# Kernel optimization log

Measured on AMD Instinct MI355X. Metric: run time of the kernel, lower is better.

The kernel has to match this reference:

```python
import jax, jax.numpy as jnp
import numpy as np

HEADS = 16
HEAD_DIM = 64
EMB = HEADS * HEAD_DIM
MAX_REL = 512
B, L = 4, 1024


def _rel_indices(length_q, length_k):
    # Shaw-style clipped relative distance indices into the embeddings table
    dist = jnp.arange(length_k)[None, :] - jnp.arange(length_q)[:, None]
    return jnp.clip(dist, -MAX_REL, MAX_REL) + MAX_REL  # [Lq, Lk] in [0, 2*MAX_REL]


def setup_inputs() -> dict:
    key = jax.random.key(0)
    ks = jax.random.split(key, 16)
    d = {
        "query": jax.random.normal(ks[0], (B, L, EMB), jnp.float32),
        "key": jax.random.normal(ks[1], (B, L, EMB), jnp.float32),
        "value": jax.random.normal(ks[2], (B, L, EMB), jnp.float32),
        "mask": jnp.ones((B, 1, L, L), jnp.int32),
        # per-head Linear(head_dims, head_dims) weights stored torch-style [out, in]
        "Wq": jax.random.normal(ks[3], (HEAD_DIM, HEAD_DIM), jnp.float32) / np.sqrt(HEAD_DIM),
        "bq": jax.random.normal(ks[4], (HEAD_DIM,), jnp.float32) * 0.02,
        "Wk": jax.random.normal(ks[5], (HEAD_DIM, HEAD_DIM), jnp.float32) / np.sqrt(HEAD_DIM),
        "bk": jax.random.normal(ks[6], (HEAD_DIM,), jnp.float32) * 0.02,
        "Wv": jax.random.normal(ks[7], (HEAD_DIM, HEAD_DIM), jnp.float32) / np.sqrt(HEAD_DIM),
        "bv": jax.random.normal(ks[8], (HEAD_DIM,), jnp.float32) * 0.02,
        "Wfc": jax.random.normal(ks[9], (EMB, EMB), jnp.float32) / np.sqrt(EMB),
        "bfc": jax.random.normal(ks[10], (EMB,), jnp.float32) * 0.02,
        "rel_k_table": jax.random.normal(ks[11], (2 * MAX_REL + 1, HEAD_DIM), jnp.float32) * 0.02,
        "rel_v_table": jax.random.normal(ks[12], (2 * MAX_REL + 1, HEAD_DIM), jnp.float32) * 0.02,
    }
    return d


def reference(query, key, value, mask, Wq, bq, Wk, bk, Wv, bv, Wfc, bfc, rel_k_table, rel_v_table):
    b, lq, _ = query.shape
    lk = key.shape[1]
    # split heads then per-head linear projections (torch Linear: x @ W.T + b)
    q = query.reshape(b, lq, HEADS, HEAD_DIM) @ Wq.T + bq
    k = key.reshape(b, lk, HEADS, HEAD_DIM) @ Wk.T + bk
    v = value.reshape(b, lk, HEADS, HEAD_DIM) @ Wv.T + bv

    score = jnp.einsum('bqhd,bkhd->bhqk', q, k)  # [B,H,Lq,Lk]
    score = jnp.where(mask == 0, jnp.float32(-1e20), score)

    idx = _rel_indices(lq, lk)
    a_key = rel_k_table[idx]    # [Lq, Lk, D]
    a_val = rel_v_table[idx]    # [Lq, Lk, D]
    score = score + jnp.einsum('blhd,lrd->bhlr', q, a_key)

    attn = jax.nn.softmax(score / np.sqrt(HEAD_DIM), axis=-1)

    out = jnp.einsum('bhqv,bvhd->bqhd', attn, v)
    # original: einsum('brhl,hld->bhrd', attn[b,h,q,k], a_val[q,k,d]) -> [b,q,h,d]
    out = out + jnp.einsum('bhql,qld->bqhd', attn, a_val)
    out = out.reshape(b, lq, EMB)
    return out @ Wfc.T + bfc
```

## Files before the change

kernel.cpp:

```cpp
#include <hip/hip_runtime.h>
#include <hip/hip_bf16.h>
#include <hip/hip_fp16.h>

#define SEQ 1024
#define HEADS 16
#define HDIM 64
#define EMB 1024
#define TQ 32
#define KQ 256
#define PBA_S 264
#define PBB_S 328
#define RELK_ROWS 1040
#define RELV_S 1064

typedef __bf16 bf16x8 __attribute__((ext_vector_type(8)));
typedef float floatx4 __attribute__((ext_vector_type(4)));
typedef unsigned short u16x4 __attribute__((ext_vector_type(4)));

#if __has_builtin(__builtin_amdgcn_exp2f)
#define EXP2F(x) __builtin_amdgcn_exp2f(x)
#else
#define EXP2F(x) exp2f(x)
#endif

#define QSCALE 0.18033688011112042f

static __device__ __forceinline__ unsigned short f2bu(float f) {
    __bf16 h = (__bf16)f;
    return __builtin_bit_cast(unsigned short, h);
}
static __device__ __forceinline__ float b2f(unsigned short u) {
    unsigned v = ((unsigned)u) << 16;
    return __builtin_bit_cast(float, v);
}

__global__ __launch_bounds__(256) void sa_proj_kernel(
    const float* __restrict__ qin, const float* __restrict__ kin,
    const float* __restrict__ vin,
    const unsigned short* __restrict__ wqb, const unsigned short* __restrict__ wkb,
    const unsigned short* __restrict__ wvb,
    const float* __restrict__ bq, const float* __restrict__ bk,
    const float* __restrict__ bv_,
    unsigned short* __restrict__ qb, unsigned short* __restrict__ kb,
    unsigned short* __restrict__ vtb,
    const unsigned* __restrict__ part, unsigned* __restrict__ flags) {
    const int t = threadIdx.x;
    if (blockIdx.x == 0 && blockIdx.y == 0 && t < 4) {
        unsigned f = 0xFFFFFFFFu;
        for (int i = 0; i < 64; ++i) f &= part[t * 64 + i];
        flags[t] = f;
    }
    const int w = t >> 6, lane = t & 63;
    const int quad = lane >> 4, l16 = lane & 15;
    const int which = blockIdx.y;
    const int bx = blockIdx.x;
    const int r0 = (bx >> 2) * 16;
    const int h = (bx & 3) * 4 + w;
    const int bidx = r0 >> 10;
    const int l0 = r0 & 1023;
    const float* x = (which == 0) ? qin : (which == 1) ? kin : vin;
    const unsigned short* Wb = (which == 0) ? wqb : (which == 1) ? wkb : wvb;
    const float* bias = (which == 0) ? bq : (which == 1) ? bk : bv_;

    bf16x8 wf[4][2];
#pragma unroll
    for (int dt = 0; dt < 4; ++dt)
#pragma unroll
        for (int ks = 0; ks < 2; ++ks)
            wf[dt][ks] = *(const bf16x8*)(Wb + (size_t)(dt * 16 + l16) * 64 + ks * 32 + quad * 8);

    bf16x8 xf[2];
#pragma unroll
    for (int ks = 0; ks < 2; ++ks) {
        const float* xp = x + (size_t)(r0 + l16) * EMB + h * 64 + ks * 32 + quad * 8;
        float4 lo = *(const float4*)xp;
        float4 hi = *(const float4*)(xp + 4);
        unsigned short px[8];
        px[0] = f2bu(lo.x); px[1] = f2bu(lo.y); px[2] = f2bu(lo.z); px[3] = f2bu(lo.w);
        px[4] = f2bu(hi.x); px[5] = f2bu(hi.y); px[6] = f2bu(hi.z); px[7] = f2bu(hi.w);
        xf[ks] = *(bf16x8*)px;
    }
    const int bh = bidx * HEADS + h;

    if (which < 2) {
        float biasd[4];
#pragma unroll
        for (int dt = 0; dt < 4; ++dt) biasd[dt] = bias[dt * 16 + l16];
        const float sc = (which == 0) ? QSCALE : 1.0f;
        unsigned short* dst = (which == 0) ? qb : kb;
        floatx4 acc[4];
#pragma unroll
        for (int dt = 0; dt < 4; ++dt) acc[dt] = floatx4{0.f, 0.f, 0.f, 0.f};
#pragma unroll
        for (int dt = 0; dt < 4; ++dt)
#pragma unroll
            for (int ks = 0; ks < 2; ++ks)
                acc[dt] = __builtin_amdgcn_mfma_f32_16x16x32_bf16(xf[ks], wf[dt][ks], acc[dt], 0, 0, 0);
#pragma unroll
        for (int dt = 0; dt < 4; ++dt)
#pragma unroll
            for (int i = 0; i < 4; ++i) {
                const int lr = l0 + quad * 4 + i;
                float val = (acc[dt][i] + biasd[dt]) * sc;
                dst[((size_t)bh * SEQ + lr) * 64 + dt * 16 + l16] = f2bu(val);
            }
    } else {
        float biasv[4][4];
#pragma unroll
        for (int dt = 0; dt < 4; ++dt)
#pragma unroll
            for (int i = 0; i < 4; ++i) biasv[dt][i] = bias[dt * 16 + quad * 4 + i];
        floatx4 acc[4];
#pragma unroll
        for (int dt = 0; dt < 4; ++dt) acc[dt] = floatx4{0.f, 0.f, 0.f, 0.f};
#pragma unroll
        for (int dt = 0; dt < 4; ++dt)
#pragma unroll
            for (int ks = 0; ks < 2; ++ks)
                acc[dt] = __builtin_amdgcn_mfma_f32_16x16x32_bf16(wf[dt][ks], xf[ks], acc[dt], 0, 0, 0);
#pragma unroll
        for (int dt = 0; dt < 4; ++dt)
#pragma unroll
            for (int i = 0; i < 4; ++i) {
                const int d = dt * 16 + quad * 4 + i;
                float val = acc[dt][i] + biasv[dt][i];
                vtb[((size_t)bh * 64 + d) * SEQ + l0 + l16] = f2bu(val);
            }
    }
}

#define NW (1024 * 1024)
#define NRK (RELK_ROWS * 64)
#define NRV (64 * RELV_S)
#define NWP (3 * 4096)
#define CONV_BLOCKS ((NW + NRK + NRV + NWP) / 256)
__global__ __launch_bounds__(256) void sa_prep_kernel(
    const float* __restrict__ Wfc, const float* __restrict__ relk,
    const float* __restrict__ relv,
    const float* __restrict__ Wq, const float* __restrict__ Wk,
    const float* __restrict__ Wv, const int* __restrict__ mask,
    unsigned short* __restrict__ wfcb, unsigned short* __restrict__ relkb,
    unsigned short* __restrict__ relvtb,
    unsigned short* __restrict__ wqb, unsigned short* __restrict__ wkb,
    unsigned short* __restrict__ wvb, unsigned* __restrict__ part) {
    const int bx = blockIdx.x;
    const int t = threadIdx.x;
    if (bx < CONV_BLOCKS) {
        int i = bx * 256 + t;
        if (i < NW) {
            wfcb[i] = f2bu(Wfc[i]);
        } else if (i < NW + NRK) {
            int j = i - NW;
            int r = j >> 6, d = j & 63;
            relkb[j] = (r <= 1024) ? f2bu(relk[r * 64 + d]) : 0;
        } else if (i < NW + NRK + NRV) {
            int j = i - NW - NRK;
            int d = j / RELV_S, c = j - d * RELV_S;
            relvtb[j] = (c <= 1024) ? f2bu(relv[c * 64 + d]) : 0;
        } else {
            int j = i - NW - NRK - NRV;
            int which = j >> 12, e = j & 4095;
            const float* src = (which == 0) ? Wq : (which == 1) ? Wk : Wv;
            unsigned short* dst = (which == 0) ? wqb : (which == 1) ? wkb : wvb;
            dst[e] = f2bu(src[e]);
        }
    } else {
        const int mb = bx - CONV_BLOCKS;
        const int b = mb >> 6, chunk = mb & 63;
        const int4* p = (const int4*)(mask + (size_t)b * (SEQ * SEQ) + chunk * 16384);
        int ok = 1;
#pragma unroll
        for (int i = 0; i < 16; ++i) {
            int4 v = p[t + i * 256];
            ok &= (v.x != 0 && v.y != 0 && v.z != 0 && v.w != 0) ? 1 : 0;
        }
        unsigned long long bal = __ballot(ok);
        __shared__ unsigned wok[4];
        if ((t & 63) == 0) wok[t >> 6] = (bal == ~0ull) ? 1u : 0u;
        __syncthreads();
        if (t == 0)
            part[b * 64 + chunk] = (wok[0] & wok[1] & wok[2] & wok[3]) ? 0xFFFFFFFFu : 0u;
    }
}

__global__ __launch_bounds__(512, 6) void sa_attn_kernel(
    const unsigned short* __restrict__ qb, const unsigned short* __restrict__ kb,
    const unsigned short* __restrict__ vtb, const int* __restrict__ mask,
    const unsigned short* __restrict__ relkb, const unsigned short* __restrict__ relvtb,
    const unsigned* __restrict__ flags, unsigned short* __restrict__ aob) {
    __shared__ __align__(16) unsigned short PbA[TQ * PBA_S];
    __shared__ __align__(16) unsigned short PbB[TQ * PBB_S];

    const int tid = threadIdx.x;
    const int w = tid >> 6, lane = tid & 63;
    const int quad = lane >> 4, l16 = lane & 15;
    const int bid = blockIdx.x;
    const int qt = bid & 31;
    const int bh = bid >> 5;
    const int q0 = qt * TQ;
    const int b = bh >> 4, h = bh & 15;
    const bool mfull = (flags[b] == 0xFFFFFFFFu);

    bf16x8 aq[2][2];
#pragma unroll
    for (int rt = 0; rt < 2; ++rt) {
        const unsigned short* qrow = qb + ((size_t)bh * SEQ + q0 + rt * 16 + l16) * 64;
        aq[rt][0] = *(const bf16x8*)(qrow + quad * 8);
        aq[rt][1] = *(const bf16x8*)(qrow + 32 + quad * 8);
    }

    const int rtF = w & 1;
    const int dq = w >> 1;
    const unsigned short* vrow = vtb + ((size_t)bh * 64 + dq * 16 + l16) * SEQ;
    const unsigned short* rbase = relvtb + (size_t)(dq * 16 + l16) * RELV_S;
    const float rv0 = b2f(rbase[0]);
    const float rv1 = b2f(rbase[1024]);
    unsigned short ob[8];
#pragma unroll
    for (int j = 0; j < 8; ++j) ob[j] = 0x3F80;
    const bf16x8 onesf = *(bf16x8*)ob;

    floatx4 OaccA = {0.f, 0.f, 0.f, 0.f};
    floatx4 OaccB = {0.f, 0.f, 0.f, 0.f};
    floatx4 dnm = {0.f, 0.f, 0.f, 0.f};
    floatx4 tl = {0.f, 0.f, 0.f, 0.f};
    floatx4 th = {0.f, 0.f, 0.f, 0.f};

    for (int qu = 0; qu < 4; ++qu) {
        const int k0 = qu * KQ;
        const bool clipped = (k0 - (q0 + 31) < -512) || (k0 + 255 - q0 > 512);
        const int cmin = min(512, max(-512, k0 - (q0 + 31))) + 512;
        const int cmax = min(512, max(-512, k0 + 255 - q0)) + 512;
        const int BASE = cmin & ~15;

        __syncthreads();

        {
            const int ct_lo = cmin >> 4, ct_hi = cmax >> 4;
            for (int ct = ct_lo + w; ct <= ct_hi; ct += 8) {
                bf16x8 bf0 = *(const bf16x8*)(relkb + (size_t)(ct * 16 + l16) * 64 + quad * 8);
                bf16x8 bf1 = *(const bf16x8*)(relkb + (size_t)(ct * 16 + l16) * 64 + 32 + quad * 8);
                floatx4 r0 = {0.f, 0.f, 0.f, 0.f}, r1 = {0.f, 0.f, 0.f, 0.f};
                r0 = __builtin_amdgcn_mfma_f32_16x16x32_bf16(bf0, aq[0][0], r0, 0, 0, 0);
                r0 = __builtin_amdgcn_mfma_f32_16x16x32_bf16(bf1, aq[0][1], r0, 0, 0, 0);
                r1 = __builtin_amdgcn_mfma_f32_16x16x32_bf16(bf0, aq[1][0], r1, 0, 0, 0);
                r1 = __builtin_amdgcn_mfma_f32_16x16x32_bf16(bf1, aq[1][1], r1, 0, 0, 0);
                const int co = ct * 16 + quad * 4 - BASE;
                u16x4 p0, p1;
#pragma unroll
                for (int i = 0; i < 4; ++i) { p0[i] = f2bu(r0[i]); p1[i] = f2bu(r1[i]); }
                *(u16x4*)&PbB[(size_t)l16 * PBB_S + co] = p0;
                *(u16x4*)&PbB[(size_t)(16 + l16) * PBB_S + co] = p1;
            }
        }
        __syncthreads();

        const int kc = w;
        floatx4 acc[2][2];
#pragma unroll
        for (int rt = 0; rt < 2; ++rt)
#pragma unroll
            for (int tt = 0; tt < 2; ++tt) acc[rt][tt] = floatx4{0.f, 0.f, 0.f, 0.f};
#pragma unroll
        for (int tt = 0; tt < 2; ++tt) {
            const unsigned short* krow = kb + ((size_t)bh * SEQ + k0 + kc * 32 + tt * 16 + l16) * 64;
            bf16x8 kf0 = *(const bf16x8*)(krow + quad * 8);
            bf16x8 kf1 = *(const bf16x8*)(krow + 32 + quad * 8);
            acc[0][tt] = __builtin_amdgcn_mfma_f32_16x16x32_bf16(kf0, aq[0][0], acc[0][tt], 0, 0, 0);
            acc[0][tt] = __builtin_amdgcn_mfma_f32_16x16x32_bf16(kf1, aq[0][1], acc[0][tt], 0, 0, 0);
            acc[1][tt] = __builtin_amdgcn_mfma_f32_16x16x32_bf16(kf0, aq[1][0], acc[1][tt], 0, 0, 0);
            acc[1][tt] = __builtin_amdgcn_mfma_f32_16x16x32_bf16(kf1, aq[1][1], acc[1][tt], 0, 0, 0);
        }
        u16x4 pk[2][2];
        if (mfull) {
            if (!clipped) {
#pragma unroll
                for (int rt = 0; rt < 2; ++rt) {
                    const unsigned short* rsrow = &PbB[(size_t)(rt * 16 + l16) * PBB_S];
                    const int cb = k0 + kc * 32 - (q0 + rt * 16 + l16) + 512 - BASE;
#pragma unroll
                    for (int tt = 0; tt < 2; ++tt)
#pragma unroll
                        for (int i = 0; i < 4; ++i) {
                            float s = acc[rt][tt][i] + b2f(rsrow[cb + tt * 16 + quad * 4 + i]);
                            pk[rt][tt][i] = f2bu(EXP2F(s));
                        }
                }
            } else {
#pragma unroll
                for (int rt = 0; rt < 2; ++rt) {
                    const unsigned short* rsrow = &PbB[(size_t)(rt * 16 + l16) * PBB_S];
                    const int cb = k0 + kc * 32 - (q0 + rt * 16 + l16) + 512;
#pragma unroll
                    for (int tt = 0; tt < 2; ++tt)
#pragma unroll
                        for (int i = 0; i < 4; ++i) {
                            const int c = cb + tt * 16 + quad * 4 + i;
                            const int r = min(1024, max(0, c));
                            float s = acc[rt][tt][i] + b2f(rsrow[r - BASE]);
                            pk[rt][tt][i] = f2bu(EXP2F(s));
                        }
                }
            }
        } else {
#pragma unroll
            for (int rt = 0; rt < 2; ++rt) {
                const unsigned short* rsrow = &PbB[(size_t)(rt * 16 + l16) * PBB_S];
                const int q = q0 + rt * 16 + l16;
                const int cb = k0 + kc * 32 - q + 512;
                const int* mrow = mask + (size_t)b * (SEQ * SEQ) + (size_t)q * SEQ;
#pragma unroll
                for (int tt = 0; tt < 2; ++tt)
#pragma unroll
                    for (int i = 0; i < 4; ++i) {
                        const int k = k0 + kc * 32 + tt * 16 + quad * 4 + i;
                        const int c = cb + tt * 16 + quad * 4 + i;
                        const int r = min(1024, max(0, c));
                        float s = acc[rt][tt][i] + b2f(rsrow[r - BASE]);
                        int m = mrow[k];
                        s = (m == 0) ? -1e20f : s;
                        pk[rt][tt][i] = f2bu(EXP2F(s));
                    }
            }
        }
#pragma unroll
        for (int rt = 0; rt < 2; ++rt)
#pragma unroll
            for (int tt = 0; tt < 2; ++tt)
                *(u16x4*)&PbA[(size_t)(rt * 16 + l16) * PBA_S + kc * 32 + tt * 16 + quad * 4] = pk[rt][tt];
        __syncthreads();

        for (int g = tid; g < TQ * (PBB_S / 8); g += 512) {
            int row = g / (PBB_S / 8), j = g - row * (PBB_S / 8);
            *(uint4*)&PbB[row * PBB_S + j * 8] = make_uint4(0u, 0u, 0u, 0u);
        }
        __syncthreads();

#pragma unroll
        for (int rt = 0; rt < 2; ++rt) {
            unsigned short* pbrow = &PbB[(size_t)(rt * 16 + l16) * PBB_S];
            const int cbase = k0 + kc * 32 - (q0 + rt * 16 + l16) + 512;
#pragma unroll
            for (int tt = 0; tt < 2; ++tt) {
                const int c0 = cbase + tt * 16 + quad * 4;
                if (!clipped) {
#pragma unroll
                    for (int i = 0; i < 4; ++i) pbrow[c0 + i - BASE] = pk[rt][tt][i];
                } else {
#pragma unroll
                    for (int i = 0; i < 4; ++i) {
                        const int c = c0 + i;
                        if ((unsigned)(c - 1) < 1023u) pbrow[c - BASE] = pk[rt][tt][i];
                    }
                }
            }
        }
        __syncthreads();

        {
            floatx4 accS = {0.f, 0.f, 0.f, 0.f};
            floatx4 accSI = {0.f, 0.f, 0.f, 0.f};
#pragma unroll
            for (int it = 0; it < 8; ++it) {
                const int co = it * 32 + quad * 8;
                bf16x8 ap = *(const bf16x8*)&PbA[(size_t)(rtF * 16 + l16) * PBA_S + co];
                bf16x8 bv = *(const bf16x8*)(vrow + k0 + co);
                OaccA = __builtin_amdgcn_mfma_f32_16x16x32_bf16(ap, bv, OaccA, 0, 0, 0);
                accS = __builtin_amdgcn_mfma_f32_16x16x32_bf16(ap, onesf, accS, 0, 0, 0);
            }
            const int nksB = ((cmax - BASE) >> 5) + 1;
            for (int ks = 0; ks < nksB; ++ks) {
                const int co = ks * 32 + quad * 8;
                bf16x8 ar = *(const bf16x8*)&PbB[(size_t)(rtF * 16 + l16) * PBB_S + co];
                bf16x8 br = *(const bf16x8*)(rbase + BASE + co);
                OaccB = __builtin_amdgcn_mfma_f32_16x16x32_bf16(ar, br, OaccB, 0, 0, 0);
                accSI = __builtin_amdgcn_mfma_f32_16x16x32_bf16(ar, onesf, accSI, 0, 0, 0);
            }
#pragma unroll
            for (int i = 0; i < 4; ++i) {
                dnm[i] += accS[i];
                const float tail = accS[i] - accSI[i];
                const int qi = q0 + rtF * 16 + quad * 4 + i;
                if (qi >= k0 + 512) tl[i] += tail;
                if (qi <= k0 - 257) th[i] += tail;
            }
        }
    }

#pragma unroll
    for (int i = 0; i < 4; ++i) {
        const int row = rtF * 16 + quad * 4 + i;
        const int q = q0 + row;
        const float val = (OaccA[i] + OaccB[i] + tl[i] * rv0 + th[i] * rv1) / dnm[i];
        aob[((size_t)b * SEQ + q) * EMB + h * 64 + dq * 16 + l16] = f2bu(val);
    }
}

__global__ __launch_bounds__(256, 2) void sa_fc_kernel(
    const unsigned short* __restrict__ A, const unsigned short* __restrict__ W,
    const float* __restrict__ bias, float* __restrict__ out) {
    const int t = threadIdx.x;
    const int w = t >> 6, lane = t & 63;
    const int quad = lane >> 4, l16 = lane & 15;
    const int mw = blockIdx.x * 64 + (w & 1) * 32;
    const int nw = blockIdx.y * 256 + (w >> 1) * 128;

    floatx4 acc[2][8];
#pragma unroll
    for (int mt = 0; mt < 2; ++mt)
#pragma unroll
        for (int j = 0; j < 8; ++j) acc[mt][j] = floatx4{0.f, 0.f, 0.f, 0.f};
    float bj[8];
#pragma unroll
    for (int j = 0; j < 8; ++j) bj[j] = bias[nw + j * 16 + l16];

    for (int ks = 0; ks < 32; ++ks) {
        const int co = ks * 32 + quad * 8;
        bf16x8 af0 = *(const bf16x8*)(A + (size_t)(mw + l16) * EMB + co);
        bf16x8 af1 = *(const bf16x8*)(A + (size_t)(mw + 16 + l16) * EMB + co);
#pragma unroll
        for (int j = 0; j < 8; ++j) {
            bf16x8 bf = *(const bf16x8*)(W + (size_t)(nw + j * 16 + l16) * EMB + co);
            acc[0][j] = __builtin_amdgcn_mfma_f32_16x16x32_bf16(af0, bf, acc[0][j], 0, 0, 0);
            acc[1][j] = __builtin_amdgcn_mfma_f32_16x16x32_bf16(af1, bf, acc[1][j], 0, 0, 0);
        }
    }
#pragma unroll
    for (int mt = 0; mt < 2; ++mt)
#pragma unroll
        for (int j = 0; j < 8; ++j) {
            const int col = nw + j * 16 + l16;
#pragma unroll
            for (int i = 0; i < 4; ++i) {
                const size_t row = mw + mt * 16 + quad * 4 + i;
                out[row * EMB + col] = acc[mt][j][i] + bj[j];
            }
        }
}

extern "C" void kernel_launch(void* const* d_in, const int* in_sizes, int n_in,
                              void* d_out, int out_size, void* d_ws, size_t ws_size,
                              hipStream_t stream) {
    const float* query = (const float*)d_in[0];
    const float* key = (const float*)d_in[1];
    const float* value = (const float*)d_in[2];
    const int* mask = (const int*)d_in[3];
    const float* Wq = (const float*)d_in[4];
    const float* bq = (const float*)d_in[5];
    const float* Wk = (const float*)d_in[6];
    const float* bk = (const float*)d_in[7];
    const float* Wv = (const float*)d_in[8];
    const float* bv = (const float*)d_in[9];
    const float* Wfc = (const float*)d_in[10];
    const float* bfc = (const float*)d_in[11];
    const float* relk = (const float*)d_in[12];
    const float* relv = (const float*)d_in[13];
    float* out = (float*)d_out;

    char* base = (char*)d_ws;
    const size_t MB = (size_t)1 << 20;
    unsigned short* qb = (unsigned short*)(base + 0 * MB);
    unsigned short* kb = (unsigned short*)(base + 8 * MB);
    unsigned short* vtb = (unsigned short*)(base + 16 * MB);
    unsigned short* wfcb = (unsigned short*)(base + 24 * MB);
    unsigned short* relkb = (unsigned short*)(base + 26 * MB);
    unsigned short* relvtb = (unsigned short*)(base + 26 * MB + 163840);
    unsigned short* wqb = (unsigned short*)(base + 26 * MB + 327680);
    unsigned short* wkb = (unsigned short*)(base + 26 * MB + 335872);
    unsigned short* wvb = (unsigned short*)(base + 26 * MB + 344064);
    unsigned* flags = (unsigned*)(base + 26 * MB + 360448);
    unsigned* part = (unsigned*)(base + 26 * MB + 364544);
    unsigned short* aob = (unsigned short*)(base + 29 * MB);

    sa_prep_kernel<<<CONV_BLOCKS + 256, 256, 0, stream>>>(
        Wfc, relk, relv, Wq, Wk, Wv, mask, wfcb, relkb, relvtb, wqb, wkb, wvb, part);
    sa_proj_kernel<<<dim3(1024, 3), 256, 0, stream>>>(
        query, key, value, wqb, wkb, wvb, bq, bk, bv, qb, kb, vtb, part, flags);
    sa_attn_kernel<<<64 * 32, 512, 0, stream>>>(
        qb, kb, vtb, mask, relkb, relvtb, flags, aob);
    sa_fc_kernel<<<dim3(64, 4), 256, 0, stream>>>(aob, wfcb, bfc, out);
}
```

Before: 456.8 us.

## Merge prep and projection kernels; reduce mask flags inside attention kernel

Folds the weight/table conversion and mask-scan prep kernel into the projection launch as extra grid blocks, so one kernel launch and its serialization point go away. The projection now converts the per-head weights from fp32 on the fly, and the attention kernel reduces the per-chunk mask flags itself with a ballot. The score loop is restructured per row tile to cut live registers, re-reading probabilities from shared memory for the scatter. The cost is redundant weight conversion in every projection block and an extra block-level sync in attention.

Result: slower. 492.8 us (+7.9%).

```diff
diff --git a/kernel.cpp b/kernel.cpp
--- a/kernel.cpp
+++ b/kernel.cpp
@@ -34,40 +34,86 @@
     return __builtin_bit_cast(float, v);
 }
 
-__global__ __launch_bounds__(256) void sa_proj_kernel(
+#define NW (1024 * 1024)
+#define NRK (RELK_ROWS * 64)
+#define NRV (64 * RELV_S)
+#define CONVB ((NW + NRK + NRV) / 256)
+#define PREPY 1626
+__global__ __launch_bounds__(256) void sa_projprep_kernel(
     const float* __restrict__ qin, const float* __restrict__ kin,
     const float* __restrict__ vin,
-    const unsigned short* __restrict__ wqb, const unsigned short* __restrict__ wkb,
-    const unsigned short* __restrict__ wvb,
+    const float* __restrict__ Wq, const float* __restrict__ Wk,
+    const float* __restrict__ Wv,
     const float* __restrict__ bq, const float* __restrict__ bk,
     const float* __restrict__ bv_,
+    const float* __restrict__ Wfc, const float* __restrict__ relk,
+    const float* __restrict__ relv, const int* __restrict__ mask,
     unsigned short* __restrict__ qb, unsigned short* __restrict__ kb,
     unsigned short* __restrict__ vtb,
-    const unsigned* __restrict__ part, unsigned* __restrict__ flags) {
+    unsigned short* __restrict__ wfcb, unsigned short* __restrict__ relkb,
+    unsigned short* __restrict__ relvtb, unsigned* __restrict__ part) {
+    __shared__ unsigned wok[4];
     const int t = threadIdx.x;
-    if (blockIdx.x == 0 && blockIdx.y == 0 && t < 4) {
-        unsigned f = 0xFFFFFFFFu;
-        for (int i = 0; i < 64; ++i) f &= part[t * 64 + i];
-        flags[t] = f;
-    }
+    const int which = blockIdx.y;
+    const int bx = blockIdx.x;
+
+    if (bx >= 1024) {
+        const int gidx = (bx - 1024) + which * PREPY;
+        if (gidx < CONVB) {
+            int i = gidx * 256 + t;
+            if (i < NW) {
+                wfcb[i] = f2bu(Wfc[i]);
+            } else if (i < NW + NRK) {
+                int j = i - NW;
+                int r = j >> 6, d = j & 63;
+                relkb[j] = (r <= 1024) ? f2bu(relk[r * 64 + d]) : 0;
+            } else {
+                int j = i - NW - NRK;
+                int d = j / RELV_S, c = j - d * RELV_S;
+                relvtb[j] = (c <= 1024) ? f2bu(relv[c * 64 + d]) : 0;
+            }
+        } else if (gidx < CONVB + 256) {
+            const int mb = gidx - CONVB;
+            const int b = mb >> 6, chunk = mb & 63;
+            const int4* p = (const int4*)(mask + (size_t)b * (SEQ * SEQ) + chunk * 16384);
+            int ok = 1;
+#pragma unroll
+            for (int i = 0; i < 16; ++i) {
+                int4 v = p[t + i * 256];
+                ok &= (v.x != 0 && v.y != 0 && v.z != 0 && v.w != 0) ? 1 : 0;
+            }
+            unsigned long long bal = __ballot(ok);
+            if ((t & 63) == 0) wok[t >> 6] = (bal == ~0ull) ? 1u : 0u;
+            __syncthreads();
+            if (t == 0)
+                part[b * 64 + chunk] = (wok[0] & wok[1] & wok[2] & wok[3]) ? 0xFFFFFFFFu : 0u;
+        }
+        return;
+    }
+
     const int w = t >> 6, lane = t & 63;
     const int quad = lane >> 4, l16 = lane & 15;
-    const int which = blockIdx.y;
-    const int bx = blockIdx.x;
     const int r0 = (bx >> 2) * 16;
     const int h = (bx & 3) * 4 + w;
     const int bidx = r0 >> 10;
     const int l0 = r0 & 1023;
     const float* x = (which == 0) ? qin : (which == 1) ? kin : vin;
-    const unsigned short* Wb = (which == 0) ? wqb : (which == 1) ? wkb : wvb;
+    const float* Wsrc = (which == 0) ? Wq : (which == 1) ? Wk : Wv;
     const float* bias = (which == 0) ? bq : (which == 1) ? bk : bv_;
 
     bf16x8 wf[4][2];
 #pragma unroll
     for (int dt = 0; dt < 4; ++dt)
 #pragma unroll
-        for (int ks = 0; ks < 2; ++ks)
-            wf[dt][ks] = *(const bf16x8*)(Wb + (size_t)(dt * 16 + l16) * 64 + ks * 32 + quad * 8);
+        for (int ks = 0; ks < 2; ++ks) {
+            const float* wp = Wsrc + (size_t)(dt * 16 + l16) * 64 + ks * 32 + quad * 8;
+            float4 lo = *(const float4*)wp;
+            float4 hi = *(const float4*)(wp + 4);
+            unsigned short pw[8];
+            pw[0] = f2bu(lo.x); pw[1] = f2bu(lo.y); pw[2] = f2bu(lo.z); pw[3] = f2bu(lo.w);
+            pw[4] = f2bu(hi.x); pw[5] = f2bu(hi.y); pw[6] = f2bu(hi.z); pw[7] = f2bu(hi.w);
+            wf[dt][ks] = *(bf16x8*)pw;
+        }
 
     bf16x8 xf[2];
 #pragma unroll
@@ -129,67 +175,14 @@
     }
 }
 
-#define NW (1024 * 1024)
-#define NRK (RELK_ROWS * 64)
-#define NRV (64 * RELV_S)
-#define NWP (3 * 4096)
-#define CONV_BLOCKS ((NW + NRK + NRV + NWP) / 256)
-__global__ __launch_bounds__(256) void sa_prep_kernel(
-    const float* __restrict__ Wfc, const float* __restrict__ relk,
-    const float* __restrict__ relv,
-    const float* __restrict__ Wq, const float* __restrict__ Wk,
-    const float* __restrict__ Wv, const int* __restrict__ mask,
-    unsigned short* __restrict__ wfcb, unsigned short* __restrict__ relkb,
-    unsigned short* __restrict__ relvtb,
-    unsigned short* __restrict__ wqb, unsigned short* __restrict__ wkb,
-    unsigned short* __restrict__ wvb, unsigned* __restrict__ part) {
-    const int bx = blockIdx.x;
-    const int t = threadIdx.x;
-    if (bx < CONV_BLOCKS) {
-        int i = bx * 256 + t;
-        if (i < NW) {
-            wfcb[i] = f2bu(Wfc[i]);
-        } else if (i < NW + NRK) {
-            int j = i - NW;
-            int r = j >> 6, d = j & 63;
-            relkb[j] = (r <= 1024) ? f2bu(relk[r * 64 + d]) : 0;
-        } else if (i < NW + NRK + NRV) {
-            int j = i - NW - NRK;
-            int d = j / RELV_S, c = j - d * RELV_S;
-            relvtb[j] = (c <= 1024) ? f2bu(relv[c * 64 + d]) : 0;
-        } else {
-            int j = i - NW - NRK - NRV;
-            int which = j >> 12, e = j & 4095;
-            const float* src = (which == 0) ? Wq : (which == 1) ? Wk : Wv;
-            unsigned short* dst = (which == 0) ? wqb : (which == 1) ? wkb : wvb;
-            dst[e] = f2bu(src[e]);
-        }
-    } else {
-        const int mb = bx - CONV_BLOCKS;
-        const int b = mb >> 6, chunk = mb & 63;
-        const int4* p = (const int4*)(mask + (size_t)b * (SEQ * SEQ) + chunk * 16384);
-        int ok = 1;
-#pragma unroll
-        for (int i = 0; i < 16; ++i) {
-            int4 v = p[t + i * 256];
-            ok &= (v.x != 0 && v.y != 0 && v.z != 0 && v.w != 0) ? 1 : 0;
-        }
-        unsigned long long bal = __ballot(ok);
-        __shared__ unsigned wok[4];
-        if ((t & 63) == 0) wok[t >> 6] = (bal == ~0ull) ? 1u : 0u;
-        __syncthreads();
-        if (t == 0)
-            part[b * 64 + chunk] = (wok[0] & wok[1] & wok[2] & wok[3]) ? 0xFFFFFFFFu : 0u;
-    }
-}
-
 __global__ __launch_bounds__(512, 6) void sa_attn_kernel(
     const unsigned short* __restrict__ qb, const unsigned short* __restrict__ kb,
     const unsigned short* __restrict__ vtb, const int* __restrict__ mask,
     const unsigned short* __restrict__ relkb, const unsigned short* __restrict__ relvtb,
-    const unsigned* __restrict__ flags, unsigned short* __restrict__ aob) {
+    const unsigned* __restrict__ part, unsigned short* __restrict__ aob) {
     __shared__ __align__(16) unsigned short PbA[TQ * PBA_S];
     __shared__ __align__(16) unsigned short PbB[TQ * PBB_S];
+    __shared__ unsigned sflag;
 
     const int tid = threadIdx.x;
     const int w = tid >> 6, lane = tid & 63;
@@ -199,7 +192,12 @@
     const int bh = bid >> 5;
     const int q0 = qt * TQ;
     const int b = bh >> 4, h = bh & 15;
-    const bool mfull = (flags[b] == 0xFFFFFFFFu);
+
+    if (tid < 64) {
+        unsigned f = part[(bid >> 9) * 64 + tid];
+        unsigned long long bal = __ballot(f != 0u);
+        if (tid == 0) sflag = (bal == ~0ull) ? 1u : 0u;
+    }
 
     bf16x8 aq[2][2];
 #pragma unroll
@@ -226,6 +224,10 @@
     floatx4 tl = {0.f, 0.f, 0.f, 0.f};
     floatx4 th = {0.f, 0.f, 0.f, 0.f};
 
+    __syncthreads();
+    const bool mfull = (sflag != 0u);
+    const int kc = w;
+
     for (int qu = 0; qu < 4; ++qu) {
         const int k0 = qu * KQ;
         const bool clipped = (k0 - (q0 + 31) < -512) || (k0 + 255 - q0 > 512);
@@ -233,7 +235,7 @@
         const int cmax = min(512, max(-512, k0 + 255 - q0)) + 512;
         const int BASE = cmin & ~15;
 
-        __syncthreads();
+        if (qu) __syncthreads();
 
         {
             const int ct_lo = cmin >> 4, ct_hi = cmax >> 4;
@@ -255,79 +257,64 @@
         }
         __syncthreads();
 
-        const int kc = w;
-        floatx4 acc[2][2];
-#pragma unroll
-        for (int rt = 0; rt < 2; ++rt)
-#pragma unroll
-            for (int tt = 0; tt < 2; ++tt) acc[rt][tt] = floatx4{0.f, 0.f, 0.f, 0.f};
+        bf16x8 kf[2][2];
 #pragma unroll
         for (int tt = 0; tt < 2; ++tt) {
             const unsigned short* krow = kb + ((size_t)bh * SEQ + k0 + kc * 32 + tt * 16 + l16) * 64;
-            bf16x8 kf0 = *(const bf16x8*)(krow + quad * 8);
-            bf16x8 kf1 = *(const bf16x8*)(krow + 32 + quad * 8);
-            acc[0][tt] = __builtin_amdgcn_mfma_f32_16x16x32_bf16(kf0, aq[0][0], acc[0][tt], 0, 0, 0);
-            acc[0][tt] = __builtin_amdgcn_mfma_f32_16x16x32_bf16(kf1, aq[0][1], acc[0][tt], 0, 0, 0);
-            acc[1][tt] = __builtin_amdgcn_mfma_f32_16x16x32_bf16(kf0, aq[1][0], acc[1][tt], 0, 0, 0);
-            acc[1][tt] = __builtin_amdgcn_mfma_f32_16x16x32_bf16(kf1, aq[1][1], acc[1][tt], 0, 0, 0);
-        }
-        u16x4 pk[2][2];
-        if (mfull) {
-            if (!clipped) {
-#pragma unroll
-                for (int rt = 0; rt < 2; ++rt) {
-                    const unsigned short* rsrow = &PbB[(size_t)(rt * 16 + l16) * PBB_S];
-                    const int cb = k0 + kc * 32 - (q0 + rt * 16 + l16) + 512 - BASE;
-#pragma unroll
-                    for (int tt = 0; tt < 2; ++tt)
-#pragma unroll
-                        for (int i = 0; i < 4; ++i) {
-                            float s = acc[rt][tt][i] + b2f(rsrow[cb + tt * 16 + quad * 4 + i]);
-                            pk[rt][tt][i] = f2bu(EXP2F(s));
-                        }
+            kf[tt][0] = *(const bf16x8*)(krow + quad * 8);
+            kf[tt][1] = *(const bf16x8*)(krow + 32 + quad * 8);
+        }
+#pragma unroll
+        for (int rt = 0; rt < 2; ++rt) {
+            floatx4 a0 = {0.f, 0.f, 0.f, 0.f}, a1 = {0.f, 0.f, 0.f, 0.f};
+            a0 = __builtin_amdgcn_mfma_f32_16x16x32_bf16(kf[0][0], aq[rt][0], a0, 0, 0, 0);
+            a0 = __builtin_amdgcn_mfma_f32_16x16x32_bf16(kf[0][1], aq[rt][1], a0, 0, 0, 0);
+            a1 = __builtin_amdgcn_mfma_f32_16x16x32_bf16(kf[1][0], aq[rt][0], a1, 0, 0, 0);
+            a1 = __builtin_amdgcn_mfma_f32_16x16x32_bf16(kf[1][1], aq[rt][1], a1, 0, 0, 0);
+            const unsigned short* rsrow = &PbB[(size_t)(rt * 16 + l16) * PBB_S];
+            const int q = q0 + rt * 16 + l16;
+            const int cb = k0 + kc * 32 - q + 512;
+            u16x4 pa0, pa1;
+            if (mfull) {
+                if (!clipped) {
+#pragma unroll
+                    for (int i = 0; i < 4; ++i) {
+                        pa0[i] = f2bu(EXP2F(a0[i] + b2f(rsrow[cb + quad * 4 + i - BASE])));
+                        pa1[i] = f2bu(EXP2F(a1[i] + b2f(rsrow[cb + 16 + quad * 4 + i - BASE])));
+                    }
+                } else {
+#pragma unroll
+                    for (int i = 0; i < 4; ++i) {
+                        const int c0 = cb + quad * 4 + i;
+                        const int c1 = c0 + 16;
+                        const int r0i = min(1024, max(0, c0));
+                        const int r1i = min(1024, max(0, c1));
+                        pa0[i] = f2bu(EXP2F(a0[i] + b2f(rsrow[r0i - BASE])));
+                        pa1[i] = f2bu(EXP2F(a1[i] + b2f(rsrow[r1i - BASE])));
+                    }
                 }
             } else {
-#pragma unroll
-                for (int rt = 0; rt < 2; ++rt) {
-                    const unsigned short* rsrow = &PbB[(size_t)(rt * 16 + l16) * PBB_S];
-                    const int cb = k0 + kc * 32 - (q0 + rt * 16 + l16) + 512;
-#pragma unroll
-                    for (int tt = 0; tt < 2; ++tt)
-#pragma unroll
-                        for (int i = 0; i < 4; ++i) {
-                            const int c = cb + tt * 16 + quad * 4 + i;
-                            const int r = min(1024, max(0, c));
-                            float s = acc[rt][tt][i] + b2f(rsrow[r - BASE]);
-                            pk[rt][tt][i] = f2bu(EXP2F(s));
-                        }
+                const int* mrow = mask + (size_t)b * (SEQ * SEQ) + (size_t)q * SEQ;
+#pragma unroll
+                for (int i = 0; i < 4; ++i) {
+                    const int k0i = k0 + kc * 32 + quad * 4 + i;
+                    const int k1i = k0i + 16;
+                    const int c0 = cb + quad * 4 + i;
+                    const int c1 = c0 + 16;
+                    const int r0i = min(1024, max(0, c0));
+                    const int r1i = min(1024, max(0, c1));
+                    float s0 = a0[i] + b2f(rsrow[r0i - BASE]);
+                    float s1 = a1[i] + b2f(rsrow[r1i - BASE]);
+                    s0 = (mrow[k0i] == 0) ? -1e20f : s0;
+                    s1 = (mrow[k1i] == 0) ? -1e20f : s1;
+                    pa0[i] = f2bu(EXP2F(s0));
+                    pa1[i] = f2bu(EXP2F(s1));
                 }
             }
-        } else {
-#pragma unroll
-            for (int rt = 0; rt < 2; ++rt) {
-                const unsigned short* rsrow = &PbB[(size_t)(rt * 16 + l16) * PBB_S];
-                const int q = q0 + rt * 16 + l16;
-                const int cb = k0 + kc * 32 - q + 512;
-                const int* mrow = mask + (size_t)b * (SEQ * SEQ) + (size_t)q * SEQ;
-#pragma unroll
-                for (int tt = 0; tt < 2; ++tt)
-#pragma unroll
-                    for (int i = 0; i < 4; ++i) {
-                        const int k = k0 + kc * 32 + tt * 16 + quad * 4 + i;
-                        const int c = cb + tt * 16 + quad * 4 + i;
-                        const int r = min(1024, max(0, c));
-                        float s = acc[rt][tt][i] + b2f(rsrow[r - BASE]);
-                        int m = mrow[k];
-                        s = (m == 0) ? -1e20f : s;
-                        pk[rt][tt][i] = f2bu(EXP2F(s));
-                    }
-            }
-        }
-#pragma unroll
-        for (int rt = 0; rt < 2; ++rt)
-#pragma unroll
-            for (int tt = 0; tt < 2; ++tt)
-                *(u16x4*)&PbA[(size_t)(rt * 16 + l16) * PBA_S + kc * 32 + tt * 16 + quad * 4] = pk[rt][tt];
+            unsigned short* parow = &PbA[(size_t)(rt * 16 + l16) * PBA_S + kc * 32];
+            *(u16x4*)(parow + quad * 4) = pa0;
+            *(u16x4*)(parow + 16 + quad * 4) = pa1;
+        }
         __syncthreads();
 
         for (int g = tid; g < TQ * (PBB_S / 8); g += 512) {
@@ -339,18 +326,20 @@
 #pragma unroll
         for (int rt = 0; rt < 2; ++rt) {
             unsigned short* pbrow = &PbB[(size_t)(rt * 16 + l16) * PBB_S];
+            const unsigned short* parow = &PbA[(size_t)(rt * 16 + l16) * PBA_S + kc * 32];
             const int cbase = k0 + kc * 32 - (q0 + rt * 16 + l16) + 512;
 #pragma unroll
             for (int tt = 0; tt < 2; ++tt) {
+                u16x4 pr = *(const u16x4*)(parow + tt * 16 + quad * 4);
                 const int c0 = cbase + tt * 16 + quad * 4;
                 if (!clipped) {
 #pragma unroll
-                    for (int i = 0; i < 4; ++i) pbrow[c0 + i - BASE] = pk[rt][tt][i];
+                    for (int i = 0; i < 4; ++i) pbrow[c0 + i - BASE] = pr[i];
                 } else {
 #pragma unroll
                     for (int i = 0; i < 4; ++i) {
                         const int c = c0 + i;
-                        if ((unsigned)(c - 1) < 1023u) pbrow[c - BASE] = pk[rt][tt][i];
+                        if ((unsigned)(c - 1) < 1023u) pbrow[c - BASE] = pr[i];
                     }
                 }
             }
@@ -465,18 +454,13 @@
     unsigned short* wfcb = (unsigned short*)(base + 24 * MB);
     unsigned short* relkb = (unsigned short*)(base + 26 * MB);
     unsigned short* relvtb = (unsigned short*)(base + 26 * MB + 163840);
-    unsigned short* wqb = (unsigned short*)(base + 26 * MB + 327680);
-    unsigned short* wkb = (unsigned short*)(base + 26 * MB + 335872);
-    unsigned short* wvb = (unsigned short*)(base + 26 * MB + 344064);
-    unsigned* flags = (unsigned*)(base + 26 * MB + 360448);
-    unsigned* part = (unsigned*)(base + 26 * MB + 364544);
+    unsigned* part = (unsigned*)(base + 26 * MB + 327680);
     unsigned short* aob = (unsigned short*)(base + 29 * MB);
 
-    sa_prep_kernel<<<CONV_BLOCKS + 256, 256, 0, stream>>>(
-        Wfc, relk, relv, Wq, Wk, Wv, mask, wfcb, relkb, relvtb, wqb, wkb, wvb, part);
-    sa_proj_kernel<<<dim3(1024, 3), 256, 0, stream>>>(
-        query, key, value, wqb, wkb, wvb, bq, bk, bv, qb, kb, vtb, part, flags);
+    sa_projprep_kernel<<<dim3(1024 + PREPY, 3), 256, 0, stream>>>(
+        query, key, value, Wq, Wk, Wv, bq, bk, bv,
+        Wfc, relk, relv, mask, qb, kb, vtb, wfcb, relkb, relvtb, part);
     sa_attn_kernel<<<64 * 32, 512, 0, stream>>>(
-        qb, kb, vtb, mask, relkb, relvtb, flags, aob);
+        qb, kb, vtb, mask, relkb, relvtb, part, aob);
     sa_fc_kernel<<<dim3(64, 4), 256, 0, stream>>>(aob, wfcb, bfc, out);
 }
```
